# Performance work log

Hardware: AMD Instinct MI355X
Metric: run time of the kernel (lower is better)

## Reference

```python
import jax, jax.numpy as jnp
import numpy as np

INPUT_DIM = 1024
OUTPUT_DIM = 1024
NUM_EXPERTS = 8
HIDDEN_DIM = 64
N_TOKENS = 8192


def setup_inputs() -> dict:
    key = jax.random.key(0)
    ks = jax.random.split(key, 7)
    s_in = 1.0 / np.sqrt(INPUT_DIM)
    s_h = 1.0 / np.sqrt(HIDDEN_DIM)
    return {
        "x": jax.random.normal(ks[0], (N_TOKENS, INPUT_DIM), dtype=jnp.float32),
        # per-expert Linear(input_dim, output_dim): weight [E, out, in], bias [E, out]
        "We": jax.random.uniform(ks[1], (NUM_EXPERTS, OUTPUT_DIM, INPUT_DIM), minval=-s_in, maxval=s_in, dtype=jnp.float32),
        "be": jax.random.uniform(ks[2], (NUM_EXPERTS, OUTPUT_DIM), minval=-s_in, maxval=s_in, dtype=jnp.float32),
        # gating: Linear(input_dim, hidden) -> ReLU -> Linear(hidden, num_experts)
        "Wg1": jax.random.uniform(ks[3], (HIDDEN_DIM, INPUT_DIM), minval=-s_in, maxval=s_in, dtype=jnp.float32),
        "bg1": jax.random.uniform(ks[4], (HIDDEN_DIM,), minval=-s_in, maxval=s_in, dtype=jnp.float32),
        "Wg2": jax.random.uniform(ks[5], (NUM_EXPERTS, HIDDEN_DIM), minval=-s_h, maxval=s_h, dtype=jnp.float32),
        "bg2": jax.random.uniform(ks[6], (NUM_EXPERTS,), minval=-s_h, maxval=s_h, dtype=jnp.float32),
    }


def reference(x, We, be, Wg1, bg1, Wg2, bg2):
    # gating network
    h = jax.nn.relu(x @ Wg1.T + bg1)                 # [N, H]
    gate_scores = h @ Wg2.T + bg2                    # [N, E]
    gate_weights = jax.nn.softmax(gate_scores, axis=-1)
    top2_weights, top2_indices = jax.lax.top_k(gate_weights, 2)  # [N, 2]
    # dense expert compute: every expert on every token (faithful to source)
    expert_outputs = jnp.einsum('ni,eoi->neo', x, We) + be       # [N, E, D_out]
    # gather top-2 expert outputs and combine
    gathered = jnp.take_along_axis(expert_outputs, top2_indices[:, :, None], axis=1)  # [N, 2, D_out]
    output = jnp.sum(gathered * top2_weights[:, :, None], axis=1)  # [N, D_out]
    return output, gate_weights, top2_indices
```

## Files before the change

### kernel.cpp

```cpp
#include <hip/hip_runtime.h>
#include <stdint.h>

#define N_TOKENS 8192
#define IN_DIM   1024
#define OUT_DIM  1024
#define NE       8
#define HID      64

typedef __attribute__((ext_vector_type(8))) short bf16x8;
typedef __attribute__((ext_vector_type(4))) float f32x4;

__device__ __forceinline__ unsigned short f2bf(float f) {
    unsigned int b = __float_as_uint(f);
    b += 0x7fffu + ((b >> 16) & 1u);
    return (unsigned short)(b >> 16);
}
__device__ __forceinline__ float bf2f(unsigned short u) {
    return __uint_as_float(((unsigned int)u) << 16);
}

__device__ __forceinline__ void gl16(const unsigned short* g, unsigned short* l) {
    __builtin_amdgcn_global_load_lds(
        (const __attribute__((address_space(1))) unsigned int*)g,
        (__attribute__((address_space(3))) unsigned int*)l,
        16, 0, 0);
}

__global__ __launch_bounds__(256) void conv_bf16(
    const float* __restrict__ src, unsigned short* __restrict__ dst, int n4)
{
    int i = blockIdx.x * 256 + threadIdx.x;
    const int stride = gridDim.x * 256;
    for (; i < n4; i += stride) {
        float4 v = ((const float4*)src)[i];
        ushort4 h;
        h.x = f2bf(v.x); h.y = f2bf(v.y); h.z = f2bf(v.z); h.w = f2bf(v.w);
        ((ushort4*)dst)[i] = h;
    }
}

__global__ __launch_bounds__(256) void split_wg1(
    const float* __restrict__ src, unsigned short* __restrict__ hi,
    unsigned short* __restrict__ lo, int n4)
{
    int i = blockIdx.x * 256 + threadIdx.x;
    if (i >= n4) return;
    float4 v = ((const float4*)src)[i];
    ushort4 h, l;
    h.x = f2bf(v.x); l.x = f2bf(v.x - bf2f(h.x));
    h.y = f2bf(v.y); l.y = f2bf(v.y - bf2f(h.y));
    h.z = f2bf(v.z); l.z = f2bf(v.z - bf2f(h.z));
    h.w = f2bf(v.w); l.w = f2bf(v.w - bf2f(h.w));
    ((ushort4*)hi)[i] = h;
    ((ushort4*)lo)[i] = l;
}

__global__ __launch_bounds__(256) void gating_kernel(
    const float* __restrict__ x, unsigned short* __restrict__ xh_out,
    const unsigned short* __restrict__ wg1h, const unsigned short* __restrict__ wg1l,
    const float* __restrict__ bg1,
    const float* __restrict__ Wg2, const float* __restrict__ bg2,
    float* __restrict__ out_gw, float* __restrict__ out_idx,
    int* __restrict__ counts, int* __restrict__ bucket_tok, float* __restrict__ bucket_w)
{
    __shared__ unsigned short Xh_s[64 * 32], Xl_s[64 * 32];
    __shared__ unsigned short Gh_s[64 * 32], Gl_s[64 * 32];
    __shared__ float Hs[64][68];
    __shared__ float W2s[NE][HID];
    __shared__ float b2s[NE];

    const int tid  = threadIdx.x;
    const int wv   = tid >> 6;
    const int lane = tid & 63;
    const int t0   = blockIdx.x * 64;

    for (int i = tid; i < NE * HID; i += 256) W2s[i >> 6][i & 63] = Wg2[i];
    if (tid < NE) b2s[tid] = bg2[tid];

    const int r = tid >> 2;
    const int c = tid & 3;
    const float* xsrc = x + (size_t)(t0 + r) * IN_DIM + c * 8;
    unsigned short* xdst = xh_out + (size_t)(t0 + r) * IN_DIM + c * 8;

    const unsigned short* gh_src = wg1h + (size_t)(wv * 16 + (lane >> 2)) * IN_DIM + (lane & 3) * 8;
    const unsigned short* gl_src = wg1l + (size_t)(wv * 16 + (lane >> 2)) * IN_DIM + (lane & 3) * 8;
    unsigned short* gh_dst = &Gh_s[wv * 512];
    unsigned short* gl_dst = &Gl_s[wv * 512];

    const int fr = lane & 15;
    const int kb = (lane >> 4) * 8;

    f32x4 acc[4];
#pragma unroll
    for (int mi = 0; mi < 4; ++mi) acc[mi] = (f32x4)0.0f;

    for (int k0 = 0; k0 < IN_DIM; k0 += 32) {
        float4 v0 = *(const float4*)(xsrc + k0);
        float4 v1 = *(const float4*)(xsrc + k0 + 4);
        bf16x8 xh8, xl8;
        {
            float vv[8] = {v0.x, v0.y, v0.z, v0.w, v1.x, v1.y, v1.z, v1.w};
#pragma unroll
            for (int j = 0; j < 8; ++j) {
                unsigned short h = f2bf(vv[j]);
                xh8[j] = (short)h;
                xl8[j] = (short)f2bf(vv[j] - bf2f(h));
            }
        }
        *(bf16x8*)(xdst + k0) = xh8;

        __syncthreads();
        *(bf16x8*)&Xh_s[r * 32 + c * 8] = xh8;
        *(bf16x8*)&Xl_s[r * 32 + c * 8] = xl8;
        gl16(gh_src + k0, gh_dst);
        gl16(gl_src + k0, gl_dst);
        __syncthreads();

        bf16x8 bh = *(const bf16x8*)&Gh_s[(wv * 16 + fr) * 32 + kb];
        bf16x8 bl = *(const bf16x8*)&Gl_s[(wv * 16 + fr) * 32 + kb];
#pragma unroll
        for (int mi = 0; mi < 4; ++mi) {
            bf16x8 ah = *(const bf16x8*)&Xh_s[(mi * 16 + fr) * 32 + kb];
            bf16x8 al = *(const bf16x8*)&Xl_s[(mi * 16 + fr) * 32 + kb];
            acc[mi] = __builtin_amdgcn_mfma_f32_16x16x32_bf16(ah, bh, acc[mi], 0, 0, 0);
            acc[mi] = __builtin_amdgcn_mfma_f32_16x16x32_bf16(ah, bl, acc[mi], 0, 0, 0);
            acc[mi] = __builtin_amdgcn_mfma_f32_16x16x32_bf16(al, bh, acc[mi], 0, 0, 0);
        }
    }

    const float bgv = bg1[wv * 16 + fr];
#pragma unroll
    for (int mi = 0; mi < 4; ++mi)
#pragma unroll
        for (int rg = 0; rg < 4; ++rg)
            Hs[mi * 16 + (lane >> 4) * 4 + rg][wv * 16 + fr] = fmaxf(acc[mi][rg] + bgv, 0.0f);
    __syncthreads();

    if (tid < 64) {
        const int token = t0 + tid;
        float sc[NE];
#pragma unroll
        for (int e2 = 0; e2 < NE; ++e2) {
            float s = b2s[e2];
#pragma unroll
            for (int j = 0; j < HID; ++j) s += Hs[tid][j] * W2s[e2][j];
            sc[e2] = s;
        }
        float m = sc[0];
#pragma unroll
        for (int e2 = 1; e2 < NE; ++e2) m = fmaxf(m, sc[e2]);
        float sum = 0.0f;
#pragma unroll
        for (int e2 = 0; e2 < NE; ++e2) { sc[e2] = expf(sc[e2] - m); sum += sc[e2]; }
        const float inv = 1.0f / sum;
#pragma unroll
        for (int e2 = 0; e2 < NE; ++e2) { sc[e2] *= inv; out_gw[(size_t)token * NE + e2] = sc[e2]; }

        int i1 = 0; float v1 = sc[0];
#pragma unroll
        for (int e2 = 1; e2 < NE; ++e2) if (sc[e2] > v1) { v1 = sc[e2]; i1 = e2; }
        int i2 = -1; float v2 = -1e30f;
#pragma unroll
        for (int e2 = 0; e2 < NE; ++e2) {
            if (e2 == i1) continue;
            if (i2 < 0 || sc[e2] > v2) { v2 = sc[e2]; i2 = e2; }
        }
        out_idx[(size_t)token * 2 + 0] = (float)i1;
        out_idx[(size_t)token * 2 + 1] = (float)i2;

        const unsigned long long lmask = (1ull << tid) - 1ull;
#pragma unroll
        for (int e2 = 0; e2 < NE; ++e2) {
            unsigned long long m1 = __ballot(i1 == e2);
            unsigned long long m2 = __ballot(i2 == e2);
            int c1 = __popcll(m1), c2 = __popcll(m2);
            int base = 0;
            if (tid == 0 && (c1 + c2) > 0) base = atomicAdd(&counts[e2 * 16], c1 + c2);
            base = __shfl(base, 0);
            if (i1 == e2) {
                int pos = base + __popcll(m1 & lmask);
                bucket_tok[e2 * N_TOKENS + pos] = token * 2 + 0;
                bucket_w  [e2 * N_TOKENS + pos] = v1;
            }
            if (i2 == e2) {
                int pos = base + c1 + __popcll(m2 & lmask);
                bucket_tok[e2 * N_TOKENS + pos] = token * 2 + 1;
                bucket_w  [e2 * N_TOKENS + pos] = v2;
            }
        }
    }
}

#define BM 128
#define KS 32

__global__ __launch_bounds__(256) void expert_gemm(
    const unsigned short* __restrict__ xh, const unsigned short* __restrict__ wh,
    const float* __restrict__ be, const int* __restrict__ counts,
    const int* __restrict__ bucket_tok, const float* __restrict__ bucket_w,
    float* __restrict__ tmp)
{
    const int e  = blockIdx.z;
    const int tt = blockIdx.y;
    const int ot = blockIdx.x;
    const int cnt = counts[e * 16];
    if (tt * BM >= cnt) return;

    __shared__ unsigned short Xh[BM * KS], Wh[BM * KS];
    __shared__ int   slt[BM];
    __shared__ float wts[BM];

    const int tid  = threadIdx.x;
    const int wv   = tid >> 6;
    const int lane = tid & 63;

    if (tid < BM) {
        int idx = tt * BM + tid;
        slt[tid] = (idx < cnt) ? bucket_tok[e * N_TOKENS + idx] : -1;
        wts[tid] = (idx < cnt) ? bucket_w [e * N_TOKENS + idx] : 0.0f;
    }
    __syncthreads();

    const int l4 = lane >> 2;
    const int kq = lane & 3;
    const int rA = wv * 32 + l4;
    const int s0 = slt[rA], s1 = slt[rA + 16];
    const int tk0 = (s0 < 0) ? 0 : (s0 >> 1);
    const int tk1 = (s1 < 0) ? 0 : (s1 >> 1);

    const unsigned short* sX0 = xh + (size_t)tk0 * IN_DIM + kq * 8;
    const unsigned short* sX1 = xh + (size_t)tk1 * IN_DIM + kq * 8;
    const unsigned short* sW0 = wh + ((size_t)e * OUT_DIM + ot * BM + rA) * IN_DIM + kq * 8;
    const unsigned short* sW1 = sW0 + (size_t)16 * IN_DIM;

    unsigned short* dX = &Xh[wv * 1024];
    unsigned short* dW = &Wh[wv * 1024];

    const int wm = wv >> 1, wn = wv & 1;
    const int fr = lane & 15;
    const int kb = (lane >> 4) * 8;

    f32x4 acc[4][4];
#pragma unroll
    for (int mi = 0; mi < 4; ++mi)
#pragma unroll
        for (int ni = 0; ni < 4; ++ni) acc[mi][ni] = (f32x4)0.0f;

    for (int k0 = 0; k0 < IN_DIM; k0 += KS) {
        __syncthreads();
        gl16(sX0 + k0, dX);  gl16(sX1 + k0, dX + 512);
        gl16(sW0 + k0, dW);  gl16(sW1 + k0, dW + 512);
        __syncthreads();

        bf16x8 ah[4], bh[4];
#pragma unroll
        for (int mi = 0; mi < 4; ++mi)
            ah[mi] = *(const bf16x8*)&Xh[(wm * 64 + mi * 16 + fr) * KS + kb];
#pragma unroll
        for (int ni = 0; ni < 4; ++ni)
            bh[ni] = *(const bf16x8*)&Wh[(wn * 64 + ni * 16 + fr) * KS + kb];
#pragma unroll
        for (int mi = 0; mi < 4; ++mi)
#pragma unroll
            for (int ni = 0; ni < 4; ++ni)
                acc[mi][ni] = __builtin_amdgcn_mfma_f32_16x16x32_bf16(ah[mi], bh[ni], acc[mi][ni], 0, 0, 0);
    }

    const int colbase = ot * BM + wn * 64;
    float bias[4];
#pragma unroll
    for (int ni = 0; ni < 4; ++ni) bias[ni] = be[(size_t)e * OUT_DIM + colbase + ni * 16 + fr];

#pragma unroll
    for (int mi = 0; mi < 4; ++mi) {
#pragma unroll
        for (int r = 0; r < 4; ++r) {
            const int ri = wm * 64 + mi * 16 + (lane >> 4) * 4 + r;
            const int s  = slt[ri];
            if (s < 0) continue;
            const float w = wts[ri];
            float* orow = tmp + (size_t)s * OUT_DIM + colbase;
#pragma unroll
            for (int ni = 0; ni < 4; ++ni)
                orow[ni * 16 + fr] = w * (acc[mi][ni][r] + bias[ni]);
        }
    }
}

__global__ __launch_bounds__(256) void combine_kernel(
    const float* __restrict__ tmp, float* __restrict__ out, int n4)
{
    int i = blockIdx.x * 256 + threadIdx.x;
    const int stride = gridDim.x * 256;
    const int row4 = OUT_DIM / 4;
    for (; i < n4; i += stride) {
        int t  = i / row4;
        int d4 = i - t * row4;
        float4 a = ((const float4*)tmp)[(size_t)(2 * t)     * row4 + d4];
        float4 b = ((const float4*)tmp)[(size_t)(2 * t + 1) * row4 + d4];
        float4 o;
        o.x = a.x + b.x; o.y = a.y + b.y; o.z = a.z + b.z; o.w = a.w + b.w;
        ((float4*)out)[i] = o;
    }
}

extern "C" void kernel_launch(void* const* d_in, const int* in_sizes, int n_in,
                              void* d_out, int out_size, void* d_ws, size_t ws_size,
                              hipStream_t stream) {
    const float* x   = (const float*)d_in[0];
    const float* We  = (const float*)d_in[1];
    const float* be  = (const float*)d_in[2];
    const float* Wg1 = (const float*)d_in[3];
    const float* bg1 = (const float*)d_in[4];
    const float* Wg2 = (const float*)d_in[5];
    const float* bg2 = (const float*)d_in[6];

    float* out     = (float*)d_out;
    float* out_gw  = out + (size_t)N_TOKENS * OUT_DIM;
    float* out_idx = out_gw + (size_t)N_TOKENS * NE;

    char* ws = (char*)d_ws;
    int*   counts = (int*)ws;
    int*   btok   = (int*)(ws + 1024);
    float* bw     = (float*)(ws + 1024 + 262144);
    unsigned short* xh   = (unsigned short*)(ws + 525312);
    unsigned short* wh   = xh + (size_t)N_TOKENS * IN_DIM;
    unsigned short* wg1h = wh + (size_t)NE * OUT_DIM * IN_DIM;
    unsigned short* wg1l = wg1h + (size_t)HID * IN_DIM;
    float* tmp = (float*)(wg1l + (size_t)HID * IN_DIM);

    hipMemsetAsync(counts, 0, 1024, stream);

    split_wg1<<<64, 256, 0, stream>>>(Wg1, wg1h, wg1l, (HID * IN_DIM) / 4);
    conv_bf16<<<1024, 256, 0, stream>>>(We, wh, (NE * OUT_DIM * IN_DIM) / 4);

    gating_kernel<<<N_TOKENS / 64, 256, 0, stream>>>(
        x, xh, wg1h, wg1l, bg1, Wg2, bg2, out_gw, out_idx, counts, btok, bw);

    dim3 grid(OUT_DIM / BM, N_TOKENS / BM, NE);
    expert_gemm<<<grid, 256, 0, stream>>>(xh, wh, be, counts, btok, bw, tmp);

    combine_kernel<<<2048, 256, 0, stream>>>(tmp, out, (N_TOKENS * OUT_DIM) / 4);
}
```

Measured before the change: 237.1 us.

## Register-prefetch GEMM tiles, swizzle LDS, widen K step, store bf16 intermediates

The expert GEMM now loads the next K-slice from global memory into registers while the current slice is computed, and writes tiles to LDS with an XOR swizzle to avoid bank conflicts. The K step doubles to 64 and the grid order is swapped so token tiles vary fastest. Per-slot intermediate outputs are stored as bf16 instead of fp32, halving the traffic for the write and for the combine read, at some cost in accuracy. The gating kernel also prefetches the next x chunk into registers, and the combine kernel drops its grid-stride loop for a one-shot launch.

```diff
diff --git a/kernel.cpp b/kernel.cpp
--- a/kernel.cpp
+++ b/kernel.cpp
@@ -94,9 +94,10 @@
 #pragma unroll
     for (int mi = 0; mi < 4; ++mi) acc[mi] = (f32x4)0.0f;
 
+    float4 v0 = *(const float4*)(xsrc);
+    float4 v1 = *(const float4*)(xsrc + 4);
+
     for (int k0 = 0; k0 < IN_DIM; k0 += 32) {
-        float4 v0 = *(const float4*)(xsrc + k0);
-        float4 v1 = *(const float4*)(xsrc + k0 + 4);
         bf16x8 xh8, xl8;
         {
             float vv[8] = {v0.x, v0.y, v0.z, v0.w, v1.x, v1.y, v1.z, v1.w};
@@ -114,6 +115,11 @@
         *(bf16x8*)&Xl_s[r * 32 + c * 8] = xl8;
         gl16(gh_src + k0, gh_dst);
         gl16(gl_src + k0, gl_dst);
+        {
+            const int k1 = (k0 + 32) & (IN_DIM - 1);
+            v0 = *(const float4*)(xsrc + k1);
+            v1 = *(const float4*)(xsrc + k1 + 4);
+        }
         __syncthreads();
 
         bf16x8 bh = *(const bf16x8*)&Gh_s[(wv * 16 + fr) * 32 + kb];
@@ -156,14 +162,14 @@
 #pragma unroll
         for (int e2 = 0; e2 < NE; ++e2) { sc[e2] *= inv; out_gw[(size_t)token * NE + e2] = sc[e2]; }
 
-        int i1 = 0; float v1 = sc[0];
-#pragma unroll
-        for (int e2 = 1; e2 < NE; ++e2) if (sc[e2] > v1) { v1 = sc[e2]; i1 = e2; }
-        int i2 = -1; float v2 = -1e30f;
+        int i1 = 0; float v1s = sc[0];
+#pragma unroll
+        for (int e2 = 1; e2 < NE; ++e2) if (sc[e2] > v1s) { v1s = sc[e2]; i1 = e2; }
+        int i2 = -1; float v2s = -1e30f;
 #pragma unroll
         for (int e2 = 0; e2 < NE; ++e2) {
             if (e2 == i1) continue;
-            if (i2 < 0 || sc[e2] > v2) { v2 = sc[e2]; i2 = e2; }
+            if (i2 < 0 || sc[e2] > v2s) { v2s = sc[e2]; i2 = e2; }
         }
         out_idx[(size_t)token * 2 + 0] = (float)i1;
         out_idx[(size_t)token * 2 + 1] = (float)i2;
@@ -180,33 +186,34 @@
             if (i1 == e2) {
                 int pos = base + __popcll(m1 & lmask);
                 bucket_tok[e2 * N_TOKENS + pos] = token * 2 + 0;
-                bucket_w  [e2 * N_TOKENS + pos] = v1;
+                bucket_w  [e2 * N_TOKENS + pos] = v1s;
             }
             if (i2 == e2) {
                 int pos = base + c1 + __popcll(m2 & lmask);
                 bucket_tok[e2 * N_TOKENS + pos] = token * 2 + 1;
-                bucket_w  [e2 * N_TOKENS + pos] = v2;
+                bucket_w  [e2 * N_TOKENS + pos] = v2s;
             }
         }
     }
 }
 
 #define BM 128
-#define KS 32
+#define KS 64
 
 __global__ __launch_bounds__(256) void expert_gemm(
     const unsigned short* __restrict__ xh, const unsigned short* __restrict__ wh,
     const float* __restrict__ be, const int* __restrict__ counts,
     const int* __restrict__ bucket_tok, const float* __restrict__ bucket_w,
-    float* __restrict__ tmp)
-{
+    unsigned short* __restrict__ tmp)
+{
+    const int tt = blockIdx.x;
+    const int ot = blockIdx.y;
     const int e  = blockIdx.z;
-    const int tt = blockIdx.y;
-    const int ot = blockIdx.x;
     const int cnt = counts[e * 16];
     if (tt * BM >= cnt) return;
 
-    __shared__ unsigned short Xh[BM * KS], Wh[BM * KS];
+    __shared__ unsigned short Xs[BM * KS];
+    __shared__ unsigned short Ws[BM * KS];
     __shared__ int   slt[BM];
     __shared__ float wts[BM];
 
@@ -221,24 +228,21 @@
     }
     __syncthreads();
 
-    const int l4 = lane >> 2;
-    const int kq = lane & 3;
-    const int rA = wv * 32 + l4;
-    const int s0 = slt[rA], s1 = slt[rA + 16];
-    const int tk0 = (s0 < 0) ? 0 : (s0 >> 1);
-    const int tk1 = (s1 < 0) ? 0 : (s1 >> 1);
-
-    const unsigned short* sX0 = xh + (size_t)tk0 * IN_DIM + kq * 8;
-    const unsigned short* sX1 = xh + (size_t)tk1 * IN_DIM + kq * 8;
-    const unsigned short* sW0 = wh + ((size_t)e * OUT_DIM + ot * BM + rA) * IN_DIM + kq * 8;
-    const unsigned short* sW1 = sW0 + (size_t)16 * IN_DIM;
-
-    unsigned short* dX = &Xh[wv * 1024];
-    unsigned short* dW = &Wh[wv * 1024];
+    const int srow  = wv * 32 + (lane >> 1);
+    const int khalf = lane & 1;
+    const int sx    = slt[srow];
+    const int stok  = (sx < 0) ? 0 : (sx >> 1);
+    const unsigned short* gX = xh + (size_t)stok * IN_DIM + khalf * 32;
+    const unsigned short* gW = wh + ((size_t)e * OUT_DIM + ot * BM + srow) * IN_DIM + khalf * 32;
+
+    int wofs[4];
+#pragma unroll
+    for (int cc = 0; cc < 4; ++cc)
+        wofs[cc] = srow * KS + (((khalf * 32 + cc * 8) ^ ((srow & 7) << 3)));
 
     const int wm = wv >> 1, wn = wv & 1;
-    const int fr = lane & 15;
-    const int kb = (lane >> 4) * 8;
+    const int fr  = lane & 15;
+    const int kbq = (lane >> 4);
 
     f32x4 acc[4][4];
 #pragma unroll
@@ -246,24 +250,49 @@
 #pragma unroll
         for (int ni = 0; ni < 4; ++ni) acc[mi][ni] = (f32x4)0.0f;
 
+    bf16x8 rX[4], rW[4];
+#pragma unroll
+    for (int cc = 0; cc < 4; ++cc) {
+        rX[cc] = *(const bf16x8*)(gX + cc * 8);
+        rW[cc] = *(const bf16x8*)(gW + cc * 8);
+    }
+
     for (int k0 = 0; k0 < IN_DIM; k0 += KS) {
+#pragma unroll
+        for (int cc = 0; cc < 4; ++cc) {
+            *(bf16x8*)&Xs[wofs[cc]] = rX[cc];
+            *(bf16x8*)&Ws[wofs[cc]] = rW[cc];
+        }
+        {
+            const int k1 = (k0 + KS) & (IN_DIM - 1);
+#pragma unroll
+            for (int cc = 0; cc < 4; ++cc) {
+                rX[cc] = *(const bf16x8*)(gX + k1 + cc * 8);
+                rW[cc] = *(const bf16x8*)(gW + k1 + cc * 8);
+            }
+        }
         __syncthreads();
-        gl16(sX0 + k0, dX);  gl16(sX1 + k0, dX + 512);
-        gl16(sW0 + k0, dW);  gl16(sW1 + k0, dW + 512);
+
+#pragma unroll
+        for (int ks = 0; ks < 2; ++ks) {
+            bf16x8 ah[4], bh[4];
+#pragma unroll
+            for (int mi = 0; mi < 4; ++mi) {
+                const int row = wm * 64 + mi * 16 + fr;
+                ah[mi] = *(const bf16x8*)&Xs[row * KS + ((ks * 32 + kbq * 8) ^ ((row & 7) << 3))];
+            }
+#pragma unroll
+            for (int ni = 0; ni < 4; ++ni) {
+                const int row = wn * 64 + ni * 16 + fr;
+                bh[ni] = *(const bf16x8*)&Ws[row * KS + ((ks * 32 + kbq * 8) ^ ((row & 7) << 3))];
+            }
+#pragma unroll
+            for (int mi = 0; mi < 4; ++mi)
+#pragma unroll
+                for (int ni = 0; ni < 4; ++ni)
+                    acc[mi][ni] = __builtin_amdgcn_mfma_f32_16x16x32_bf16(ah[mi], bh[ni], acc[mi][ni], 0, 0, 0);
+        }
         __syncthreads();
-
-        bf16x8 ah[4], bh[4];
-#pragma unroll
-        for (int mi = 0; mi < 4; ++mi)
-            ah[mi] = *(const bf16x8*)&Xh[(wm * 64 + mi * 16 + fr) * KS + kb];
-#pragma unroll
-        for (int ni = 0; ni < 4; ++ni)
-            bh[ni] = *(const bf16x8*)&Wh[(wn * 64 + ni * 16 + fr) * KS + kb];
-#pragma unroll
-        for (int mi = 0; mi < 4; ++mi)
-#pragma unroll
-            for (int ni = 0; ni < 4; ++ni)
-                acc[mi][ni] = __builtin_amdgcn_mfma_f32_16x16x32_bf16(ah[mi], bh[ni], acc[mi][ni], 0, 0, 0);
     }
 
     const int colbase = ot * BM + wn * 64;
@@ -274,34 +303,37 @@
 #pragma unroll
     for (int mi = 0; mi < 4; ++mi) {
 #pragma unroll
-        for (int r = 0; r < 4; ++r) {
-            const int ri = wm * 64 + mi * 16 + (lane >> 4) * 4 + r;
+        for (int r2 = 0; r2 < 4; ++r2) {
+            const int ri = wm * 64 + mi * 16 + (lane >> 4) * 4 + r2;
             const int s  = slt[ri];
             if (s < 0) continue;
             const float w = wts[ri];
-            float* orow = tmp + (size_t)s * OUT_DIM + colbase;
+            unsigned short* orow = tmp + (size_t)s * OUT_DIM + colbase;
 #pragma unroll
             for (int ni = 0; ni < 4; ++ni)
-                orow[ni * 16 + fr] = w * (acc[mi][ni][r] + bias[ni]);
+                orow[ni * 16 + fr] = f2bf(w * (acc[mi][ni][r2] + bias[ni]));
         }
     }
 }
 
 __global__ __launch_bounds__(256) void combine_kernel(
-    const float* __restrict__ tmp, float* __restrict__ out, int n4)
+    const unsigned short* __restrict__ tmp, float* __restrict__ out, int n8)
 {
     int i = blockIdx.x * 256 + threadIdx.x;
-    const int stride = gridDim.x * 256;
-    const int row4 = OUT_DIM / 4;
-    for (; i < n4; i += stride) {
-        int t  = i / row4;
-        int d4 = i - t * row4;
-        float4 a = ((const float4*)tmp)[(size_t)(2 * t)     * row4 + d4];
-        float4 b = ((const float4*)tmp)[(size_t)(2 * t + 1) * row4 + d4];
-        float4 o;
-        o.x = a.x + b.x; o.y = a.y + b.y; o.z = a.z + b.z; o.w = a.w + b.w;
-        ((float4*)out)[i] = o;
-    }
+    if (i >= n8) return;
+    const int t  = i >> 7;
+    const int d8 = (i & 127) * 8;
+    const unsigned short* a = tmp + (size_t)(2 * t) * OUT_DIM + d8;
+    const unsigned short* b = tmp + (size_t)(2 * t + 1) * OUT_DIM + d8;
+    bf16x8 av = *(const bf16x8*)a;
+    bf16x8 bv = *(const bf16x8*)b;
+    float o[8];
+#pragma unroll
+    for (int j = 0; j < 8; ++j)
+        o[j] = bf2f((unsigned short)av[j]) + bf2f((unsigned short)bv[j]);
+    float* orow = out + (size_t)t * OUT_DIM + d8;
+    *(float4*)(orow)     = make_float4(o[0], o[1], o[2], o[3]);
+    *(float4*)(orow + 4) = make_float4(o[4], o[5], o[6], o[7]);
 }
 
 extern "C" void kernel_launch(void* const* d_in, const int* in_sizes, int n_in,
@@ -327,7 +359,7 @@
     unsigned short* wh   = xh + (size_t)N_TOKENS * IN_DIM;
     unsigned short* wg1h = wh + (size_t)NE * OUT_DIM * IN_DIM;
     unsigned short* wg1l = wg1h + (size_t)HID * IN_DIM;
-    float* tmp = (float*)(wg1l + (size_t)HID * IN_DIM);
+    unsigned short* tmp  = wg1l + (size_t)HID * IN_DIM;
 
     hipMemsetAsync(counts, 0, 1024, stream);
 
@@ -337,8 +369,9 @@
     gating_kernel<<<N_TOKENS / 64, 256, 0, stream>>>(
         x, xh, wg1h, wg1l, bg1, Wg2, bg2, out_gw, out_idx, counts, btok, bw);
 
-    dim3 grid(OUT_DIM / BM, N_TOKENS / BM, NE);
+    dim3 grid(N_TOKENS / BM, OUT_DIM / BM, NE);
     expert_gemm<<<grid, 256, 0, stream>>>(xh, wh, be, counts, btok, bw, tmp);
 
-    combine_kernel<<<2048, 256, 0, stream>>>(tmp, out, (N_TOKENS * OUT_DIM) / 4);
-}
+    combine_kernel<<<(N_TOKENS * OUT_DIM / 8 + 255) / 256, 256, 0, stream>>>(
+        tmp, out, N_TOKENS * OUT_DIM / 8);
+}
```

Measured after the change: 279.8 us. 18.0% more time.
